# Kernel tuning notes

Hardware: AMD Instinct MI355X
Metric: run time of the kernel (lower is better)

Reference implementation:

```python
import jax, jax.numpy as jnp
import numpy as np

EPS = 1e-5
NB, NP, NA, NROT = 16, 1024, 12, 60
C0, C1 = 64, 128
CIN, CFEAT, COUT = 256, 512, 256


def _bn(x, g, b):
    # training-mode BatchNorm1d: stats over batch (+ spatial) dims, channel dim 1
    axes = (0,) if x.ndim == 2 else (0, 2)
    m = x.mean(axis=axes, keepdims=True)
    v = x.var(axis=axes, keepdims=True)
    sh = [1] * x.ndim; sh[1] = -1
    return (x - m) * jax.lax.rsqrt(v + EPS) * g.reshape(sh) + b.reshape(sh)


def _hat(v):  # (n,3) -> (n,3,3) skew-symmetric
    z = jnp.zeros_like(v[:, 0])
    return jnp.stack([z, -v[:, 2], v[:, 1],
                      v[:, 2], z, -v[:, 0],
                      -v[:, 1], v[:, 0], z], axis=-1).reshape(-1, 3, 3)


def _exp_so3(v):  # Rodrigues formula, (n,3) -> (n,3,3)
    theta = jnp.linalg.norm(v, axis=-1, keepdims=True)  # (n,1)
    k = v / jnp.where(theta < 1e-8, 1.0, theta)
    K = _hat(k)
    s = jnp.sin(theta)[..., None]
    c = (1.0 - jnp.cos(theta))[..., None]
    I = jnp.eye(3, dtype=v.dtype)
    return I + s * K + c * (K @ K)


def _pointnet(xyz, feats, W, b, g, bb):
    # PointnetSO3Conv: concat xyz (expanded over anchors) with feats, 1x1 conv, max over points
    nb, _, npts, na = feats.shape
    x = jnp.concatenate([jnp.broadcast_to(xyz[:, :, :, None], (nb, 3, npts, na)), feats], axis=1)
    y = jnp.einsum('oc,bcpa->bopa', W, x) + b[None, :, None, None]
    y = y.max(axis=2)  # max over points -> (nb, o, na)
    return jax.nn.relu(_bn(y, g, bb))


def setup_inputs() -> dict:
    key = jax.random.key(0)
    ks = iter(jax.random.split(key, 64))
    def nrm(shape, s=0.1):
        return jax.random.normal(next(ks), shape, dtype=jnp.float32) * s
    d = {
        'xyz0': nrm((NB, 3, NP), 1.0),
        'feats0': nrm((NB, C0, NP, NA), 1.0),
        'xyz1': nrm((NB, 3, NP), 1.0),
        'feats1': nrm((NB, C1, NP, NA), 1.0),
        'trace_idx': jax.random.randint(next(ks), (NA, NROT), 0, NA),
        'anchors': nrm((NROT, 3, 3), 1.0),
        'pn0_W': nrm((C0, C0 + 3)), 'pn0_b': nrm((C0,)), 'pn0_g': jnp.ones((C0,), jnp.float32), 'pn0_bb': jnp.zeros((C0,), jnp.float32),
        'pn1_W': nrm((C1, C1 + 3)), 'pn1_b': nrm((C1,)), 'pn1_g': jnp.ones((C1,), jnp.float32), 'pn1_bb': jnp.zeros((C1,), jnp.float32),
        'lin_W': nrm((CIN, C0 + C1)), 'lin_b': nrm((CIN,)), 'lin_g': jnp.ones((CIN,), jnp.float32), 'lin_bb': jnp.zeros((CIN,), jnp.float32),
        'feat_W': nrm((CFEAT, CIN * NA)), 'feat_b': nrm((CFEAT,)), 'feat_g': jnp.ones((CFEAT,), jnp.float32), 'feat_bb': jnp.zeros((CFEAT,), jnp.float32),
        'att_W1': nrm((128, CFEAT)), 'att_b1': nrm((128,)), 'att_g': jnp.ones((128,), jnp.float32), 'att_bb': jnp.zeros((128,), jnp.float32),
        'att_W2': nrm((1, 128)), 'att_b2': nrm((1,)),
        'reg_W1': nrm((128, CFEAT)), 'reg_b1': nrm((128,)), 'reg_g': jnp.ones((128,), jnp.float32), 'reg_bb': jnp.zeros((128,), jnp.float32),
        'reg_W2': nrm((7, 128)), 'reg_b2': nrm((7,)),
        'out_W1': nrm((CFEAT, CFEAT)), 'out_b1': nrm((CFEAT,)), 'out_g': jnp.ones((CFEAT,), jnp.float32), 'out_bb': jnp.zeros((CFEAT,), jnp.float32),
        'out_W2': nrm((COUT, CFEAT)), 'out_b2': nrm((COUT,)),
    }
    return d


def reference(xyz0, feats0, xyz1, feats1, trace_idx, anchors,
              pn0_W, pn0_b, pn0_g, pn0_bb, pn1_W, pn1_b, pn1_g, pn1_bb,
              lin_W, lin_b, lin_g, lin_bb, feat_W, feat_b, feat_g, feat_bb,
              att_W1, att_b1, att_g, att_bb, att_W2, att_b2,
              reg_W1, reg_b1, reg_g, reg_bb, reg_W2, reg_b2,
              out_W1, out_b1, out_g, out_bb, out_W2, out_b2):
    nb = feats0.shape[0]
    # _pooling: per-level pointnet + BN + relu, concat, pn_linear + pn_bn
    p0 = _pointnet(xyz0, feats0, pn0_W, pn0_b, pn0_g, pn0_bb)
    p1 = _pointnet(xyz1, feats1, pn1_W, pn1_b, pn1_g, pn1_bb)
    x = jnp.concatenate([p0, p1], axis=1)                                   # (nb, 192, na)
    x = _bn(jnp.einsum('oc,bca->boa', lin_W, x) + lin_b[None, :, None], lin_g, lin_bb)  # (nb,256,na)
    # gather trace_idx_ori and flatten channel x anchor dims
    x = x[:, :, trace_idx].reshape(nb, CIN * NA, NROT)                      # (nb,3072,60)
    xf = jax.nn.relu(_bn(jnp.einsum('oc,bca->boa', feat_W, x) + feat_b[None, :, None], feat_g, feat_bb))  # (nb,512,60)
    h = jax.nn.relu(_bn(jnp.einsum('oc,bca->boa', reg_W1, xf) + reg_b1[None, :, None], reg_g, reg_bb))
    residual = (jnp.einsum('oc,bca->boa', reg_W2, h) + reg_b2[None, :, None]).transpose(0, 2, 1)  # (nb,60,7)
    res_D = residual[:, :, :3] / jnp.linalg.norm(residual[:, :, :3], axis=-1, keepdims=True)
    res_N = (jax.nn.sigmoid(residual[:, :, 3]) - 0.5) * jnp.pi / 5
    res_V = res_D * res_N[..., None]
    res_R = _exp_so3(res_V.reshape(-1, 3)).reshape(nb, NROT, 3, 3)
    res_T = residual[:, :, 4:]
    pred_R = jnp.einsum('tij,btjk->btik', anchors, res_R)
    # attention head + softmax over 60 rotations
    a = jax.nn.relu(_bn(jnp.einsum('oc,bca->boa', att_W1, xf) + att_b1[None, :, None], att_g, att_bb))
    logits = (jnp.einsum('oc,bca->boa', att_W2, a) + att_b2[None, :, None])[:, 0]   # (nb,60)
    x_attn = jax.nn.softmax(logits, axis=-1)
    # max-pool over rotations + out MLP
    xm = xf.max(axis=-1)                                                    # (nb,512)
    o = jax.nn.relu(_bn(xm @ out_W1.T + out_b1, out_g, out_bb))
    x_out = o @ out_W2.T + out_b2
    return (x_out, x_attn, pred_R, res_T)
```

## Files before the change

### kernel.cpp

```cpp
#include <hip/hip_runtime.h>
#include <math.h>

#define NBATCH 16
#define NPTS   1024
#define NANG   12
#define NROTS  60
#define EPSV   1e-5f

#define WB0_OFF   0
#define WB1_OFF   3072
#define PART0_OFF 13312
#define PART1_OFF 799744
#define XF_OFF    13312
#define XM_OFF    504832
#define OACT_OFF  513024
#define XCAT_OFF  2372608
#define XLIN_OFF  2409472
#define XG_OFF    2458624
#define BRP_OFF   2458624
#define HACT_OFF  4424704
#define AACT_OFF  4547584
#define FRAW_OFF  5407744
#define FEATW_OFF 6882304

#define OUT_XOUT 0
#define OUT_ATTN 4096
#define OUT_PRED 5056
#define OUT_REST 13696

typedef short  bf16x8 __attribute__((ext_vector_type(8)));
typedef float  f32x4  __attribute__((ext_vector_type(4)));

__device__ __forceinline__ unsigned short f2bf_rne(float x){
  unsigned int u = __float_as_uint(x);
  u += 0x7FFFu + ((u >> 16) & 1u);
  return (unsigned short)(u >> 16);
}
__device__ __forceinline__ float bf2f(unsigned short h){
  return __uint_as_float(((unsigned int)h) << 16);
}

__device__ __forceinline__ bf16x8 pack8(const float* f){
  union { unsigned int u[4]; bf16x8 v; } r;
  #pragma unroll
  for (int i = 0; i < 4; i++)
    r.u[i] = __builtin_amdgcn_perm(__float_as_uint(f[2*i+1]),
                                   __float_as_uint(f[2*i]), 0x07060302u);
  return r.v;
}

__device__ __forceinline__ void stage16(const unsigned short* g, unsigned short* l){
  __builtin_amdgcn_global_load_lds((const __attribute__((address_space(1))) void*)g,
                                   (__attribute__((address_space(3))) void*)l, 16, 0, 0);
}

template<int NT>
__device__ __forceinline__ void block_stats(float v, float& m, float& var, float* sbuf){
  constexpr int NW = NT / 64;
  float s = v, s2 = v * v;
  #pragma unroll
  for (int off = 32; off; off >>= 1){
    s  += __shfl_xor(s,  off, 64);
    s2 += __shfl_xor(s2, off, 64);
  }
  const int w = threadIdx.x >> 6;
  if ((threadIdx.x & 63) == 0){ sbuf[w] = s; sbuf[NW + w] = s2; }
  __syncthreads();
  float ts = 0.f, ts2 = 0.f;
  #pragma unroll
  for (int i = 0; i < NW; i++){ ts += sbuf[i]; ts2 += sbuf[NW + i]; }
  m = ts / (float)NT;
  var = ts2 / (float)NT - m * m;
}

template<int C>
__device__ __forceinline__ void prep_wb_body(int idx, const float* __restrict__ W,
                                             unsigned short* __restrict__ Wb){
  constexpr int KPAD = C + 32;
  if (idx >= C * KPAD) return;
  const int o = idx / KPAD, k = idx % KPAD;
  float v = 0.f;
  if (k < C)          v = W[(size_t)o * (C + 3) + 3 + k];
  else if (k < C + 3) v = W[(size_t)o * (C + 3) + (k - C)];
  Wb[idx] = f2bf_rne(v);
}

__global__ __launch_bounds__(256) void prep_all(
    const float* __restrict__ W0, const float* __restrict__ W1,
    const float* __restrict__ FW,
    unsigned short* __restrict__ wb0, unsigned short* __restrict__ wb1,
    unsigned short* __restrict__ fw2){
  const int blk = blockIdx.x;
  if (blk < 24){
    prep_wb_body<64>(blk * 256 + threadIdx.x, W0, wb0);
  } else if (blk < 104){
    prep_wb_body<128>((blk - 24) * 256 + threadIdx.x, W1, wb1);
  } else {
    const int idx = (blk - 104) * 256 + threadIdx.x;
    const int o = idx / 3072, k = idx % 3072;
    const float x = FW[idx];
    const unsigned short hi = f2bf_rne(x);
    const unsigned short lo = f2bf_rne(x - bf2f(hi));
    fw2[(size_t)o * 6144 + k] = hi;
    fw2[(size_t)o * 6144 + 3072 + k] = lo;
  }
}

#define SROW 196
template<int C>
__device__ __forceinline__ void pn_body(
    int nchunk, int b,
    const float* __restrict__ xyz, const float* __restrict__ feats,
    const unsigned short* __restrict__ Wb, float* __restrict__ part,
    float* yb ){
  constexpr int KPAD = C + 32;
  constexpr int NFK  = C / 32;
  constexpr int MT   = C / 16;
  const int tid  = threadIdx.x;
  const int lane = tid & 63, wave = tid >> 6;
  const int g = lane >> 4, l16 = lane & 15;
  const int nbase = nchunk * 192;

  int nn[3], pp[3];
  #pragma unroll
  for (int t = 0; t < 3; t++){
    nn[t] = wave * 48 + t * 16 + l16;
    pp[t] = (nbase + nn[t]) / 12;
  }

  f32x4 acc[MT][3];
  #pragma unroll
  for (int m = 0; m < MT; m++)
    #pragma unroll
    for (int t = 0; t < 3; t++)
      acc[m][t] = (f32x4){0.f, 0.f, 0.f, 0.f};

  const float* fB = feats + (size_t)b * C * (NPTS * NANG) + nbase;

  #pragma unroll
  for (int ks = 0; ks < NFK; ks++){
    const int kb = ks * 32;
    float f[3][8];
    #pragma unroll
    for (int t = 0; t < 3; t++)
      #pragma unroll
      for (int j = 0; j < 8; j++)
        f[t][j] = fB[(size_t)(kb + g * 8 + j) * (NPTS * NANG) + nn[t]];
    bf16x8 Bf[3];
    #pragma unroll
    for (int t = 0; t < 3; t++) Bf[t] = pack8(f[t]);
    #pragma unroll
    for (int m = 0; m < MT; m++){
      const bf16x8 Af = *(const bf16x8*)(Wb + (size_t)(m * 16 + l16) * KPAD + kb + g * 8);
      #pragma unroll
      for (int t = 0; t < 3; t++)
        acc[m][t] = __builtin_amdgcn_mfma_f32_16x16x32_bf16(Af, Bf[t], acc[m][t], 0, 0, 0);
    }
  }

  {
    const int kb = C;
    bf16x8 Bf[3];
    #pragma unroll
    for (int t = 0; t < 3; t++){
      float f[8];
      #pragma unroll
      for (int j = 0; j < 8; j++) f[j] = 0.f;
      if (g == 0){
        #pragma unroll
        for (int j = 0; j < 3; j++)
          f[j] = xyz[(size_t)(b * 3 + j) * NPTS + pp[t]];
      }
      Bf[t] = pack8(f);
    }
    #pragma unroll
    for (int m = 0; m < MT; m++){
      const bf16x8 Af = *(const bf16x8*)(Wb + (size_t)(m * 16 + l16) * KPAD + kb + g * 8);
      #pragma unroll
      for (int t = 0; t < 3; t++)
        acc[m][t] = __builtin_amdgcn_mfma_f32_16x16x32_bf16(Af, Bf[t], acc[m][t], 0, 0, 0);
    }
  }

  #pragma unroll
  for (int m = 0; m < MT; m++){
    __syncthreads();
    #pragma unroll
    for (int t = 0; t < 3; t++)
      #pragma unroll
      for (int r = 0; r < 4; r++)
        yb[(g * 4 + r) * SROW + nn[t]] = acc[m][t][r];
    __syncthreads();
    if (tid < 192){
      const int o_l = tid / 12, a = tid % 12;
      float mx = -3.4e38f;
      #pragma unroll
      for (int pl = 0; pl < 16; pl++)
        mx = fmaxf(mx, yb[o_l * SROW + pl * 12 + a]);
      part[((size_t)(b * 64 + nchunk) * C + m * 16 + o_l) * 12 + a] = mx;
    }
  }
}

__global__ __launch_bounds__(256, 3) void pn_both(
    const float* __restrict__ xyz0, const float* __restrict__ feats0,
    const unsigned short* __restrict__ wb0, float* __restrict__ part0,
    const float* __restrict__ xyz1, const float* __restrict__ feats1,
    const unsigned short* __restrict__ wb1, float* __restrict__ part1){
  __shared__ float yb[16 * SROW];
  const int lin   = blockIdx.x + 64 * (blockIdx.y + 16 * blockIdx.z);
  const int which = lin & 1;
  const int rest  = lin >> 1;
  const int nchunk = rest & 63, b = rest >> 6;
  if (which == 0) pn_body<64> (nchunk, b, xyz0, feats0, wb0, part0, yb);
  else            pn_body<128>(nchunk, b, xyz1, feats1, wb1, part1, yb);
}

__global__ void pn_reduce_bn(const float* __restrict__ part0, const float* __restrict__ part1,
    const float* __restrict__ b0, const float* __restrict__ g0, const float* __restrict__ bb0,
    const float* __restrict__ b1, const float* __restrict__ g1, const float* __restrict__ bb1,
    float* __restrict__ xcat){
  const int ch = blockIdx.x, t = threadIdx.x;
  const int b = t / 12, a = t % 12;
  const float* part; const float *bias, *g, *bb; int o, Cl;
  if (ch < 64){ part = part0; bias = b0; g = g0; bb = bb0; o = ch;      Cl = 64;  }
  else        { part = part1; bias = b1; g = g1; bb = bb1; o = ch - 64; Cl = 128; }
  const float* pp = part + ((size_t)(b * 64) * Cl + o) * 12 + a;
  const size_t kstride = (size_t)Cl * 12;
  float v = pp[0];
  for (int k = 1; k < 64; k++) v = fmaxf(v, pp[(size_t)k * kstride]);
  v += bias[o];
  __shared__ float sbuf[8];
  float m, var;
  block_stats<192>(v, m, var, sbuf);
  float xn = (v - m) * rsqrtf(var + EPSV) * g[o] + bb[o];
  xcat[((size_t)b * 192 + ch) * 12 + a] = fmaxf(xn, 0.f);
}

__global__ void lin_bn(const float* __restrict__ xcat, const float* __restrict__ W,
    const float* __restrict__ bias, const float* __restrict__ g, const float* __restrict__ bb,
    float* __restrict__ xlin){
  const int o = blockIdx.x, t = threadIdx.x;
  const int b = t / 12, a = t % 12;
  const float* xr = xcat + (size_t)b * 2304 + a;
  const float* wr = W + (size_t)o * 192;
  float v = bias[o];
  for (int c = 0; c < 192; c++) v = fmaf(wr[c], xr[(size_t)c * 12], v);
  __shared__ float sbuf[8];
  float m, var;
  block_stats<192>(v, m, var, sbuf);
  xlin[((size_t)b * 256 + o) * 12 + a] = (v - m) * rsqrtf(var + EPSV) * g[o] + bb[o];
}

__global__ void prep_xg(const float* __restrict__ xlin, const int* __restrict__ trace,
                        unsigned short* __restrict__ Xg){
  const int n = blockIdx.x;
  const int b = n / 60, r = n % 60;
  unsigned short* row = Xg + (size_t)n * 6144;
  __shared__ int ta[12];
  if (threadIdx.x < 12) ta[threadIdx.x] = trace[threadIdx.x * 60 + r];
  __syncthreads();
  for (int i = threadIdx.x; i < 3072; i += 256){
    const int c = i / 12, a = i % 12;
    const float x = xlin[((size_t)b * 256 + c) * 12 + ta[a]];
    const unsigned short hi = f2bf_rne(x);
    const unsigned short lo = f2bf_rne(x - bf2f(hi));
    row[i] = hi;
    row[3072 + i] = lo;
  }
}

__global__ __launch_bounds__(256) void feat_mfma(
    const unsigned short* __restrict__ Wb2, const unsigned short* __restrict__ Xg,
    float* __restrict__ fraw){
  const int nblk = blockIdx.x, mblk = blockIdx.y, seg = blockIdx.z;
  const int tid = threadIdx.x;
  const int lane = tid & 63, wave = tid >> 6;
  const int g = lane >> 4, l16 = lane & 15;
  const int kA = (seg == 1) ? 3072 : 0;
  const int kB = (seg == 2) ? 3072 : 0;
  const int sw = l16 & 7;
  const int wm = wave >> 1, wn = wave & 1;

  __shared__ unsigned short As[2][64 * 64];
  __shared__ unsigned short Bs[2][64 * 64];

  int rowj[2], colj[2], ldsoff[2];
  #pragma unroll
  for (int j = 0; j < 2; j++){
    const int idx = j * 256 + wave * 64 + lane;
    rowj[j]   = idx >> 3;
    colj[j]   = ((idx & 7) ^ (rowj[j] & 7)) * 8;
    ldsoff[j] = (j * 256 + wave * 64) * 8;
  }
  const unsigned short* Agb = Wb2 + (size_t)mblk * 64 * 6144 + kA;
  const unsigned short* Bgb = Xg  + (size_t)nblk * 64 * 6144 + kB;

  f32x4 acc[2][2];
  #pragma unroll
  for (int i = 0; i < 2; i++)
    #pragma unroll
    for (int j = 0; j < 2; j++)
      acc[i][j] = (f32x4){0.f, 0.f, 0.f, 0.f};

  #pragma unroll
  for (int j = 0; j < 2; j++){
    stage16(Agb + (size_t)rowj[j] * 6144 + colj[j], &As[0][ldsoff[j]]);
    stage16(Bgb + (size_t)rowj[j] * 6144 + colj[j], &Bs[0][ldsoff[j]]);
  }
  __syncthreads();

  for (int kc = 0; kc < 3072; kc += 64){
    const int buf = (kc >> 6) & 1;
    if (kc + 64 < 3072){
      const int kn = kc + 64;
      #pragma unroll
      for (int j = 0; j < 2; j++){
        stage16(Agb + (size_t)rowj[j] * 6144 + kn + colj[j], &As[buf ^ 1][ldsoff[j]]);
        stage16(Bgb + (size_t)rowj[j] * 6144 + kn + colj[j], &Bs[buf ^ 1][ldsoff[j]]);
      }
    }
    #pragma unroll
    for (int kc2 = 0; kc2 < 64; kc2 += 32){
      const int c0 = kc2 >> 3;
      bf16x8 af[2], bfr[2];
      #pragma unroll
      for (int i = 0; i < 2; i++)
        af[i]  = *(const bf16x8*)&As[buf][(wm * 32 + i * 16 + l16) * 64 + ((c0 + g) ^ sw) * 8];
      #pragma unroll
      for (int i = 0; i < 2; i++)
        bfr[i] = *(const bf16x8*)&Bs[buf][(wn * 32 + i * 16 + l16) * 64 + ((c0 + g) ^ sw) * 8];
      #pragma unroll
      for (int i = 0; i < 2; i++)
        #pragma unroll
        for (int j = 0; j < 2; j++)
          acc[i][j] = __builtin_amdgcn_mfma_f32_16x16x32_bf16(af[i], bfr[j], acc[i][j], 0, 0, 0);
    }
    __syncthreads();
  }

  float* base = fraw + (size_t)seg * (512 * 960);
  #pragma unroll
  for (int i = 0; i < 2; i++)
    #pragma unroll
    for (int j = 0; j < 2; j++){
      const int n = nblk * 64 + wn * 32 + j * 16 + l16;
      #pragma unroll
      for (int q = 0; q < 4; q++){
        const int m = mblk * 64 + wm * 32 + i * 16 + g * 4 + q;
        base[(size_t)m * 960 + n] = acc[i][j][q];
      }
    }
}

__global__ void feat_bn(const float* __restrict__ fraw, const float* __restrict__ bias,
    const float* __restrict__ g, const float* __restrict__ bb,
    float* __restrict__ xf, float* __restrict__ xm){
  const int o = blockIdx.x, t = threadIdx.x;
  const int b = t / 60, r = t % 60;
  const size_t SS = (size_t)512 * 960;
  const size_t in = (size_t)o * 960 + t;
  float v = fraw[in] + fraw[SS + in] + fraw[2 * SS + in] + bias[o];
  __shared__ float sbuf[32];
  float m, var;
  block_stats<960>(v, m, var, sbuf);
  const float xn = fmaxf((v - m) * rsqrtf(var + EPSV) * g[o] + bb[o], 0.f);
  xf[((size_t)b * 512 + o) * 60 + r] = xn;
  __shared__ float red[960];
  red[t] = xn;
  __syncthreads();
  if (r == 0){
    float mx = red[t];
    for (int k = 1; k < 60; k++) mx = fmaxf(mx, red[t + k]);
    xm[(size_t)b * 512 + o] = mx;
  }
}

__global__ __launch_bounds__(256) void brgemm_oh1(const float* __restrict__ xf,
    const float* __restrict__ Wr, const float* __restrict__ Wa,
    float* __restrict__ brp,
    const float* __restrict__ xm, const float* __restrict__ oW1,
    const float* __restrict__ ob1, const float* __restrict__ og,
    const float* __restrict__ obb, float* __restrict__ o_act){
  const int z = blockIdx.z;
  if (z == 16){
    const int q = blockIdx.y * 4 + blockIdx.x;
    if (q >= 32) return;
    const int t = threadIdx.x;
    const int b = t & 15, j = t >> 4;
    const int oc = q * 16 + j;
    float acc = ob1[oc];
    const float* wr = oW1 + (size_t)oc * 512;
    const float* xr = xm + (size_t)b * 512;
    for (int c = 0; c < 512; c++) acc = fmaf(wr[c], xr[c], acc);
    float s = acc, s2 = acc * acc;
    #pragma unroll
    for (int off = 8; off; off >>= 1){
      s  += __shfl_xor(s,  off, 16);
      s2 += __shfl_xor(s2, off, 16);
    }
    const float m = s * (1.f / 16.f);
    const float var = s2 * (1.f / 16.f) - m * m;
    o_act[(size_t)b * 512 + oc] = fmaxf((acc - m) * rsqrtf(var + EPSV) * og[oc] + obb[oc], 0.f);
    return;
  }
  const int og_ = blockIdx.x, b = blockIdx.y;
  const int br = z >> 3, ks = z & 7;
  const float* W = br ? Wa : Wr;
  const int lane = threadIdx.x & 63, wave = threadIdx.x >> 6;
  const int obase = og_ * 32 + wave * 8;
  const int rr = lane < 60 ? lane : 0;
  const float* xb = xf + ((size_t)b * 512 + ks * 64) * 60 + rr;
  const float* wr = W + (size_t)obase * 512 + ks * 64;

  float acc[8];
  #pragma unroll
  for (int i = 0; i < 8; i++) acc[i] = 0.f;

  float cur[4], nxt[4];
  #pragma unroll
  for (int j = 0; j < 4; j++) cur[j] = xb[(size_t)j * 60];

  for (int c0 = 0; c0 < 64; c0 += 4){
    #pragma unroll
    for (int j = 0; j < 4; j++){
      int cc = c0 + 4 + j; if (cc > 63) cc = 63;
      nxt[j] = xb[(size_t)cc * 60];
    }
    #pragma unroll
    for (int j = 0; j < 4; j++)
      #pragma unroll
      for (int i = 0; i < 8; i++)
        acc[i] = fmaf(wr[(size_t)i * 512 + c0 + j], cur[j], acc[i]);
    #pragma unroll
    for (int j = 0; j < 4; j++) cur[j] = nxt[j];
  }

  if (lane < 60){
    #pragma unroll
    for (int i = 0; i < 8; i++)
      brp[(((size_t)z * NBATCH + b) * 128 + obase + i) * 60 + lane] = acc[i];
  }
}

__global__ void br_bn(const float* __restrict__ brp,
    const float* __restrict__ biasR, const float* __restrict__ gR, const float* __restrict__ bbR,
    const float* __restrict__ biasA, const float* __restrict__ gA, const float* __restrict__ bbA,
    float* __restrict__ hact, float* __restrict__ aact){
  const int o = blockIdx.x, br = blockIdx.y, t = threadIdx.x;
  const int b = t / 60, r = t % 60;
  const float* bias = br ? biasA : biasR;
  const float* g    = br ? gA    : gR;
  const float* bb   = br ? bbA   : bbR;
  float v = bias[o];
  #pragma unroll
  for (int ks = 0; ks < 8; ks++)
    v += brp[((((size_t)br * 8 + ks) * NBATCH + b) * 128 + o) * 60 + r];
  __shared__ float sbuf[32];
  float m, var;
  block_stats<960>(v, m, var, sbuf);
  float* outp = br ? aact : hact;
  outp[((size_t)b * 128 + o) * 60 + r] =
      fmaxf((v - m) * rsqrtf(var + EPSV) * g[o] + bb[o], 0.f);
}

__global__ void heads(
    const float* __restrict__ h, const float* __restrict__ rW2,
    const float* __restrict__ rb2, const float* __restrict__ anchors,
    const float* __restrict__ a, const float* __restrict__ aW2, const float* __restrict__ ab2,
    const float* __restrict__ o_act, const float* __restrict__ oW2,
    const float* __restrict__ ob2, float* __restrict__ out){
  const int b = blockIdx.x, sel = blockIdx.y, t = threadIdx.x;
  if (sel == 0){
    if (t >= 64) return;
    const int r = t < 60 ? t : 59;
    float res[7];
    #pragma unroll
    for (int j = 0; j < 7; j++) res[j] = rb2[j];
    for (int c = 0; c < 128; c++){
      const float hv = h[((size_t)b * 128 + c) * 60 + r];
      #pragma unroll
      for (int j = 0; j < 7; j++) res[j] = fmaf(rW2[j * 128 + c], hv, res[j]);
    }
    if (t >= 60) return;
    const float n = sqrtf(res[0]*res[0] + res[1]*res[1] + res[2]*res[2]);
    const float invn = 1.f / n;
    const float Nv = (1.f / (1.f + expf(-res[3])) - 0.5f) * 3.14159265358979323846f / 5.f;
    const float v0 = res[0]*invn*Nv, v1 = res[1]*invn*Nv, v2 = res[2]*invn*Nv;
    const float th = sqrtf(v0*v0 + v1*v1 + v2*v2);
    const float invt = th < 1e-8f ? 1.f : 1.f / th;
    const float k0 = v0*invt, k1 = v1*invt, k2 = v2*invt;
    const float s = sinf(th), cc = 1.f - cosf(th);
    const float K[9] = {0.f, -k2, k1,  k2, 0.f, -k0,  -k1, k0, 0.f};
    float K2[9];
    #pragma unroll
    for (int ii = 0; ii < 3; ii++)
      #pragma unroll
      for (int jj = 0; jj < 3; jj++)
        K2[ii*3+jj] = K[ii*3+0]*K[0*3+jj] + K[ii*3+1]*K[1*3+jj] + K[ii*3+2]*K[2*3+jj];
    float R[9];
    #pragma unroll
    for (int ii = 0; ii < 3; ii++)
      #pragma unroll
      for (int jj = 0; jj < 3; jj++)
        R[ii*3+jj] = (ii == jj ? 1.f : 0.f) + s * K[ii*3+jj] + cc * K2[ii*3+jj];
    const float* A = anchors + (size_t)t * 9;
    #pragma unroll
    for (int ii = 0; ii < 3; ii++)
      #pragma unroll
      for (int kk = 0; kk < 3; kk++){
        const float pv = A[ii*3+0]*R[0*3+kk] + A[ii*3+1]*R[1*3+kk] + A[ii*3+2]*R[2*3+kk];
        out[OUT_PRED + ((size_t)b * 60 + t) * 9 + ii * 3 + kk] = pv;
      }
    #pragma unroll
    for (int k = 0; k < 3; k++)
      out[OUT_REST + ((size_t)b * 60 + t) * 3 + k] = res[4 + k];
  } else if (sel == 1){
    if (t >= 64) return;
    const int r = t < 60 ? t : 59;
    float acc = ab2[0];
    for (int c = 0; c < 128; c++)
      acc = fmaf(aW2[c], a[((size_t)b * 128 + c) * 60 + r], acc);
    const float l = t < 60 ? acc : -INFINITY;
    float mx = l;
    #pragma unroll
    for (int off = 32; off; off >>= 1) mx = fmaxf(mx, __shfl_xor(mx, off, 64));
    const float e = t < 60 ? expf(l - mx) : 0.f;
    float ssum = e;
    #pragma unroll
    for (int off = 32; off; off >>= 1) ssum += __shfl_xor(ssum, off, 64);
    if (t < 60) out[OUT_ATTN + (size_t)b * 60 + t] = e / ssum;
  } else {
    const float* wr = oW2 + (size_t)t * 512;
    const float* xr = o_act + (size_t)b * 512;
    float acc = ob2[t];
    for (int c = 0; c < 512; c++) acc = fmaf(wr[c], xr[c], acc);
    out[OUT_XOUT + (size_t)b * 256 + t] = acc;
  }
}

extern "C" void kernel_launch(void* const* d_in, const int* in_sizes, int n_in,
                              void* d_out, int out_size, void* d_ws, size_t ws_size,
                              hipStream_t stream){
  const float* xyz0    = (const float*)d_in[0];
  const float* feats0  = (const float*)d_in[1];
  const float* xyz1    = (const float*)d_in[2];
  const float* feats1  = (const float*)d_in[3];
  const int*   trace   = (const int*)  d_in[4];
  const float* anchors = (const float*)d_in[5];
  const float* pn0_W  = (const float*)d_in[6];
  const float* pn0_b  = (const float*)d_in[7];
  const float* pn0_g  = (const float*)d_in[8];
  const float* pn0_bb = (const float*)d_in[9];
  const float* pn1_W  = (const float*)d_in[10];
  const float* pn1_b  = (const float*)d_in[11];
  const float* pn1_g  = (const float*)d_in[12];
  const float* pn1_bb = (const float*)d_in[13];
  const float* lin_W  = (const float*)d_in[14];
  const float* lin_b  = (const float*)d_in[15];
  const float* lin_g  = (const float*)d_in[16];
  const float* lin_bb = (const float*)d_in[17];
  const float* feat_W  = (const float*)d_in[18];
  const float* feat_b  = (const float*)d_in[19];
  const float* feat_g  = (const float*)d_in[20];
  const float* feat_bb = (const float*)d_in[21];
  const float* att_W1 = (const float*)d_in[22];
  const float* att_b1 = (const float*)d_in[23];
  const float* att_g  = (const float*)d_in[24];
  const float* att_bb = (const float*)d_in[25];
  const float* att_W2 = (const float*)d_in[26];
  const float* att_b2 = (const float*)d_in[27];
  const float* reg_W1 = (const float*)d_in[28];
  const float* reg_b1 = (const float*)d_in[29];
  const float* reg_g  = (const float*)d_in[30];
  const float* reg_bb = (const float*)d_in[31];
  const float* reg_W2 = (const float*)d_in[32];
  const float* reg_b2 = (const float*)d_in[33];
  const float* out_W1 = (const float*)d_in[34];
  const float* out_b1 = (const float*)d_in[35];
  const float* out_g  = (const float*)d_in[36];
  const float* out_bb = (const float*)d_in[37];
  const float* out_W2 = (const float*)d_in[38];
  const float* out_b2 = (const float*)d_in[39];

  float* ws  = (float*)d_ws;
  float* out = (float*)d_out;
  unsigned short* wb0 = (unsigned short*)(ws + WB0_OFF);
  unsigned short* wb1 = (unsigned short*)(ws + WB1_OFF);
  unsigned short* fw  = (unsigned short*)(ws + FEATW_OFF);
  unsigned short* xg  = (unsigned short*)(ws + XG_OFF);

  prep_all<<<6248, 256, 0, stream>>>(pn0_W, pn1_W, feat_W, wb0, wb1, fw);

  pn_both<<<dim3(64, 16, 2), 256, 0, stream>>>(xyz0, feats0, wb0, ws + PART0_OFF,
                                               xyz1, feats1, wb1, ws + PART1_OFF);

  pn_reduce_bn<<<192, 192, 0, stream>>>(ws + PART0_OFF, ws + PART1_OFF,
      pn0_b, pn0_g, pn0_bb, pn1_b, pn1_g, pn1_bb, ws + XCAT_OFF);

  lin_bn<<<256, 192, 0, stream>>>(ws + XCAT_OFF, lin_W, lin_b, lin_g, lin_bb, ws + XLIN_OFF);

  prep_xg<<<960, 256, 0, stream>>>(ws + XLIN_OFF, trace, xg);

  feat_mfma<<<dim3(15, 8, 3), 256, 0, stream>>>(fw, xg, ws + FRAW_OFF);

  feat_bn<<<512, 960, 0, stream>>>(ws + FRAW_OFF, feat_b, feat_g, feat_bb,
                                   ws + XF_OFF, ws + XM_OFF);

  brgemm_oh1<<<dim3(4, 16, 17), 256, 0, stream>>>(ws + XF_OFF, reg_W1, att_W1, ws + BRP_OFF,
      ws + XM_OFF, out_W1, out_b1, out_g, out_bb, ws + OACT_OFF);

  br_bn<<<dim3(128, 2), 960, 0, stream>>>(ws + BRP_OFF,
      reg_b1, reg_g, reg_bb, att_b1, att_g, att_bb,
      ws + HACT_OFF, ws + AACT_OFF);

  heads<<<dim3(16, 3), 256, 0, stream>>>(ws + HACT_OFF, reg_W2, reg_b2, anchors,
      ws + AACT_OFF, att_W2, att_b2, ws + OACT_OFF, out_W2, out_b2, out);
}
```

Baseline: 438.0 us.

## Split PointNet output channels across two wave groups and double-buffer feature loads

The PointNet MFMA kernel now runs 512 threads per block. Two groups of four waves each compute half of the output channels, and each group has its own LDS staging buffer for the max-reduction. Feature loads for the next K-step are prefetched into a register double buffer so global-load latency overlaps the MFMAs. This raises parallelism per block and latency hiding. The cost is higher register pressure (launch bounds 512,4) and each wave group loads the same feature values redundantly.

```diff
diff --git a/kernel.cpp b/kernel.cpp
--- a/kernel.cpp
+++ b/kernel.cpp
@@ -115,43 +115,55 @@
     float* yb ){
   constexpr int KPAD = C + 32;
   constexpr int NFK  = C / 32;
-  constexpr int MT   = C / 16;
+  constexpr int MTH  = C / 32;
   const int tid  = threadIdx.x;
-  const int lane = tid & 63, wave = tid >> 6;
+  const int lane = tid & 63, w = tid >> 6;
+  const int wo = w >> 2, wn = w & 3;
   const int g = lane >> 4, l16 = lane & 15;
+  const int o_off = wo * (C / 2);
   const int nbase = nchunk * 192;
 
   int nn[3], pp[3];
   #pragma unroll
   for (int t = 0; t < 3; t++){
-    nn[t] = wave * 48 + t * 16 + l16;
+    nn[t] = wn * 48 + t * 16 + l16;
     pp[t] = (nbase + nn[t]) / 12;
   }
 
-  f32x4 acc[MT][3];
-  #pragma unroll
-  for (int m = 0; m < MT; m++)
+  f32x4 acc[MTH][3];
+  #pragma unroll
+  for (int m = 0; m < MTH; m++)
     #pragma unroll
     for (int t = 0; t < 3; t++)
       acc[m][t] = (f32x4){0.f, 0.f, 0.f, 0.f};
 
   const float* fB = feats + (size_t)b * C * (NPTS * NANG) + nbase;
 
+  float fbuf[2][3][8];
+  #pragma unroll
+  for (int t = 0; t < 3; t++)
+    #pragma unroll
+    for (int j = 0; j < 8; j++)
+      fbuf[0][t][j] = fB[(size_t)(g * 8 + j) * (NPTS * NANG) + nn[t]];
+
   #pragma unroll
   for (int ks = 0; ks < NFK; ks++){
+    const int cur = ks & 1;
+    if (ks + 1 < NFK){
+      const int kb = (ks + 1) * 32;
+      #pragma unroll
+      for (int t = 0; t < 3; t++)
+        #pragma unroll
+        for (int j = 0; j < 8; j++)
+          fbuf[cur ^ 1][t][j] = fB[(size_t)(kb + g * 8 + j) * (NPTS * NANG) + nn[t]];
+    }
     const int kb = ks * 32;
-    float f[3][8];
-    #pragma unroll
-    for (int t = 0; t < 3; t++)
-      #pragma unroll
-      for (int j = 0; j < 8; j++)
-        f[t][j] = fB[(size_t)(kb + g * 8 + j) * (NPTS * NANG) + nn[t]];
     bf16x8 Bf[3];
     #pragma unroll
-    for (int t = 0; t < 3; t++) Bf[t] = pack8(f[t]);
-    #pragma unroll
-    for (int m = 0; m < MT; m++){
-      const bf16x8 Af = *(const bf16x8*)(Wb + (size_t)(m * 16 + l16) * KPAD + kb + g * 8);
+    for (int t = 0; t < 3; t++) Bf[t] = pack8(fbuf[cur][t]);
+    #pragma unroll
+    for (int m = 0; m < MTH; m++){
+      const bf16x8 Af = *(const bf16x8*)(Wb + (size_t)(o_off + m * 16 + l16) * KPAD + kb + g * 8);
       #pragma unroll
       for (int t = 0; t < 3; t++)
         acc[m][t] = __builtin_amdgcn_mfma_f32_16x16x32_bf16(Af, Bf[t], acc[m][t], 0, 0, 0);
@@ -174,40 +186,42 @@
       Bf[t] = pack8(f);
     }
     #pragma unroll
-    for (int m = 0; m < MT; m++){
-      const bf16x8 Af = *(const bf16x8*)(Wb + (size_t)(m * 16 + l16) * KPAD + kb + g * 8);
+    for (int m = 0; m < MTH; m++){
+      const bf16x8 Af = *(const bf16x8*)(Wb + (size_t)(o_off + m * 16 + l16) * KPAD + kb + g * 8);
       #pragma unroll
       for (int t = 0; t < 3; t++)
         acc[m][t] = __builtin_amdgcn_mfma_f32_16x16x32_bf16(Af, Bf[t], acc[m][t], 0, 0, 0);
     }
   }
 
-  #pragma unroll
-  for (int m = 0; m < MT; m++){
+  float* myb = yb + wo * (16 * SROW);
+  #pragma unroll
+  for (int m = 0; m < MTH; m++){
     __syncthreads();
     #pragma unroll
     for (int t = 0; t < 3; t++)
       #pragma unroll
       for (int r = 0; r < 4; r++)
-        yb[(g * 4 + r) * SROW + nn[t]] = acc[m][t][r];
+        myb[(g * 4 + r) * SROW + nn[t]] = acc[m][t][r];
     __syncthreads();
-    if (tid < 192){
-      const int o_l = tid / 12, a = tid % 12;
+    const int lt = tid & 255;
+    if (lt < 192){
+      const int o_l = lt / 12, a = lt % 12;
       float mx = -3.4e38f;
       #pragma unroll
       for (int pl = 0; pl < 16; pl++)
-        mx = fmaxf(mx, yb[o_l * SROW + pl * 12 + a]);
-      part[((size_t)(b * 64 + nchunk) * C + m * 16 + o_l) * 12 + a] = mx;
-    }
-  }
-}
-
-__global__ __launch_bounds__(256, 3) void pn_both(
+        mx = fmaxf(mx, myb[o_l * SROW + pl * 12 + a]);
+      part[((size_t)(b * 64 + nchunk) * C + o_off + m * 16 + o_l) * 12 + a] = mx;
+    }
+  }
+}
+
+__global__ __launch_bounds__(512, 4) void pn_both(
     const float* __restrict__ xyz0, const float* __restrict__ feats0,
     const unsigned short* __restrict__ wb0, float* __restrict__ part0,
     const float* __restrict__ xyz1, const float* __restrict__ feats1,
     const unsigned short* __restrict__ wb1, float* __restrict__ part1){
-  __shared__ float yb[16 * SROW];
+  __shared__ float yb[2 * 16 * SROW];
   const int lin   = blockIdx.x + 64 * (blockIdx.y + 16 * blockIdx.z);
   const int which = lin & 1;
   const int rest  = lin >> 1;
@@ -592,7 +606,7 @@
 
   prep_all<<<6248, 256, 0, stream>>>(pn0_W, pn1_W, feat_W, wb0, wb1, fw);
 
-  pn_both<<<dim3(64, 16, 2), 256, 0, stream>>>(xyz0, feats0, wb0, ws + PART0_OFF,
+  pn_both<<<dim3(64, 16, 2), 512, 0, stream>>>(xyz0, feats0, wb0, ws + PART0_OFF,
                                                xyz1, feats1, wb1, ws + PART1_OFF);
 
   pn_reduce_bn<<<192, 192, 0, stream>>>(ws + PART0_OFF, ws + PART1_OFF,
```

New measurement: 433.8 us. About the same (-1.0%).
